# Kernel tuning notes

Hardware: AMD Instinct MI355X
Metric: run time of the kernel (lower is better)

## Reference

```python
import jax, jax.numpy as jnp
import numpy as np

N_SUP, D = 4096, 128
N_CLASSES, SHOTS = 128, 32          # balanced episode: N_SUP = N_CLASSES * SHOTS
N_QUERY = 65536
N_BOOT = 8                          # num_bootstrap_samples


def setup_inputs() -> dict:
    key = jax.random.key(0)
    k_sup, k_q, k_boot = jax.random.split(key, 3)
    support_set_repr = jax.random.normal(k_sup, (N_SUP, D), dtype=jnp.float32)
    # balanced, sorted labels: class c owns contiguous block [c*SHOTS, (c+1)*SHOTS)
    support_labels = (jnp.arange(N_SUP, dtype=jnp.int32) // SHOTS).astype(jnp.int32)
    query_set_repr = jax.random.normal(k_q, (N_QUERY, D), dtype=jnp.float32)
    # externalized torch.randint(0, num_samples, (B, num_samples)) per class
    bootstrap_indices = jax.random.randint(
        k_boot, (N_BOOT, N_CLASSES, SHOTS), 0, SHOTS, dtype=jnp.int32)
    return {
        "support_set_repr": support_set_repr,
        "support_labels": support_labels,
        "query_set_repr": query_set_repr,
        "bootstrap_indices": bootstrap_indices,
    }


def reference(support_set_repr, support_labels, query_set_repr, bootstrap_indices):
    B, C, S = bootstrap_indices.shape
    d = support_set_repr.shape[-1]
    # labels are sorted & balanced (arange // SHOTS), so per-class gather == reshape
    class_repr = support_set_repr.reshape(C, S, d)              # [C, S, D]
    # fused bootstrap gather: [B, C, S, D]
    boot = jnp.take_along_axis(class_repr[None], bootstrap_indices[..., None], axis=2)
    protos = boot.mean(axis=2)                                   # [B, C, D]
    # cdist(q, protos, p=2) via ||q||^2 + ||p||^2 - 2 q.p
    q2 = jnp.sum(query_set_repr * query_set_repr, axis=-1)       # [NQ]
    p2 = jnp.sum(protos * protos, axis=-1)                       # [B, C]
    qp = jnp.einsum('qd,bcd->bqc', query_set_repr, protos)       # [B, NQ, C]
    d2 = q2[None, :, None] + p2[:, None, :] - 2.0 * qp
    dists = jnp.sqrt(jnp.maximum(d2, 0.0))                       # [B, NQ, C]
    # logits = mean over bootstraps of -dists
    return -dists.mean(axis=0)                                   # [NQ, C]
```

## Files before the change

### kernel.cpp

```cpp
#include <hip/hip_runtime.h>
#include <hip/hip_bf16.h>


#define DIM   128
#define NCLS  128
#define SHOTS 32
#define NB    8
#define NQ    65536

using f32x4 = __attribute__((ext_vector_type(4))) float;

__device__ __forceinline__ float fast_sqrt(float x) {
#if __has_builtin(__builtin_amdgcn_sqrtf)
  return __builtin_amdgcn_sqrtf(x);
#else
  return sqrtf(x);
#endif
}

__device__ __forceinline__ long u2l(unsigned x, unsigned y) {
  union { unsigned u[2]; long l; } v; v.u[0] = x; v.u[1] = y; return v.l;
}

__device__ __forceinline__ unsigned pack4_fp8(float a, float b, float c, float d) {
  int r = 0;
  r = __builtin_amdgcn_cvt_pk_fp8_f32(a, b, r, false);
  r = __builtin_amdgcn_cvt_pk_fp8_f32(c, d, r, true);
  return (unsigned)r;
}

__global__ __launch_bounds__(128) void proto_kernel(
    const float* __restrict__ sup, const int* __restrict__ bidx,
    unsigned char* __restrict__ pfrag, float* __restrict__ p2) {
  int bc = blockIdx.x;
  int c  = bc & (NCLS - 1);
  int d  = threadIdx.x;
  __shared__ int   sidx[SHOTS];
  __shared__ float wsum[2];
  if (d < SHOTS) sidx[d] = bidx[bc * SHOTS + d];
  __syncthreads();
  float acc = 0.f;
  const float* base = sup + c * SHOTS * DIM + d;
  #pragma unroll
  for (int s = 0; s < SHOTS; ++s) acc += base[sidx[s] * DIM];
  float proto = acc * (1.0f / 32.0f);

  int b     = bc >> 7;
  int ct    = c >> 4, l15c = c & 15;
  int kiter = d >> 5, quad = (d >> 3) & 3, j = d & 7;
  int lane  = l15c + (quad << 4);
  int addr  = ((b * 8 + ct) * 2 + (kiter >> 1)) * 1024 + lane * 16 + (kiter & 1) * 8 + j;
  int enc   = __builtin_amdgcn_cvt_pk_fp8_f32(-proto, -proto, 0, false);
  pfrag[addr] = (unsigned char)(enc & 0xff);

  float sq = proto * proto;
  #pragma unroll
  for (int off = 32; off > 0; off >>= 1) sq += __shfl_down(sq, off, 64);
  if ((d & 63) == 0) wsum[d >> 6] = sq;
  __syncthreads();
  if (d == 0) p2[bc] = (wsum[0] + wsum[1]) * 0.5f;
}

__global__ __launch_bounds__(256) void dist_kernel(
    const float* __restrict__ q, const uint4* __restrict__ pfrag,
    const float* __restrict__ p2, float* __restrict__ out) {
  int tid  = threadIdx.x;
  int w    = tid >> 6, lane = tid & 63;
  int l15  = lane & 15, quad = lane >> 4;
  int q0   = blockIdx.x << 5;

  __shared__ unsigned char aflds[8 * 512];
  __shared__ float q2s[32];

  {
    int rloc  = w * 8 + (lane >> 3);
    int chunk = lane & 7;
    const float* src = q + (size_t)(q0 + rloc) * DIM + chunk * 16;
    float4 x0 = *reinterpret_cast<const float4*>(src);
    float4 x1 = *reinterpret_cast<const float4*>(src + 4);
    float4 x2 = *reinterpret_cast<const float4*>(src + 8);
    float4 x3 = *reinterpret_cast<const float4*>(src + 12);
    float s = x0.x*x0.x + x0.y*x0.y + x0.z*x0.z + x0.w*x0.w
            + x1.x*x1.x + x1.y*x1.y + x1.z*x1.z + x1.w*x1.w
            + x2.x*x2.x + x2.y*x2.y + x2.z*x2.z + x2.w*x2.w
            + x3.x*x3.x + x3.y*x3.y + x3.z*x3.z + x3.w*x3.w;
    s += __shfl_down(s, 4, 8);
    s += __shfl_down(s, 2, 8);
    s += __shfl_down(s, 1, 8);
    if (chunk == 0) q2s[rloc] = s;

    int mt = rloc >> 4, m = rloc & 15, i = chunk >> 1, h = chunk & 1;
    unsigned char* bse = &aflds[(mt * 4 + i) * 512];
    uint2 g0, g1;
    g0.x = pack4_fp8(x0.x, x0.y, x0.z, x0.w);
    g0.y = pack4_fp8(x1.x, x1.y, x1.z, x1.w);
    g1.x = pack4_fp8(x2.x, x2.y, x2.z, x2.w);
    g1.y = pack4_fp8(x3.x, x3.y, x3.z, x3.w);
    *reinterpret_cast<uint2*>(&bse[(((h * 2 + 0) << 4) + m) * 8]) = g0;
    *reinterpret_cast<uint2*>(&bse[(((h * 2 + 1) << 4) + m) * 8]) = g1;
  }
  __syncthreads();

  long af[2][4];
  #pragma unroll
  for (int mt = 0; mt < 2; ++mt)
    #pragma unroll
    for (int k = 0; k < 4; ++k)
      af[mt][k] = *reinterpret_cast<const long*>(
          &aflds[(mt * 4 + k) * 512 + lane * 8]);

  f32x4 q2r[2];
  #pragma unroll
  for (int mt = 0; mt < 2; ++mt)
    #pragma unroll
    for (int r = 0; r < 4; ++r)
      q2r[mt][r] = q2s[mt * 16 + quad * 4 + r] * 0.5f;

  float p2v[NB][2];
  #pragma unroll
  for (int b = 0; b < NB; ++b)
    #pragma unroll
    for (int jj = 0; jj < 2; ++jj)
      p2v[b][jj] = p2[b * NCLS + (w * 2 + jj) * 16 + l15];

  f32x4 oacc[2][2];
  #pragma unroll
  for (int i = 0; i < 2; ++i)
    #pragma unroll
    for (int jj = 0; jj < 2; ++jj)
      oacc[i][jj] = (f32x4){0.f, 0.f, 0.f, 0.f};

  uint4 bufX[4], bufY[4];

  #define LOAD_B(BUF, B)                                                      \
    {                                                                         \
      _Pragma("unroll")                                                       \
      for (int jj = 0; jj < 2; ++jj) {                                        \
        int ct = w * 2 + jj;                                                  \
        const uint4* bp = pfrag + (size_t)(((B) * 8 + ct) * 2) * 64 + lane;   \
        BUF[jj * 2 + 0] = bp[0];                                              \
        BUF[jj * 2 + 1] = bp[64];                                             \
      }                                                                       \
    }

  #define COMPUTE_B(BUF, B)                                                   \
    {                                                                         \
      _Pragma("unroll")                                                       \
      for (int jj = 0; jj < 2; ++jj) {                                        \
        long b0 = u2l(BUF[jj * 2 + 0].x, BUF[jj * 2 + 0].y);                  \
        long b1 = u2l(BUF[jj * 2 + 0].z, BUF[jj * 2 + 0].w);                  \
        long b2 = u2l(BUF[jj * 2 + 1].x, BUF[jj * 2 + 1].y);                  \
        long b3 = u2l(BUF[jj * 2 + 1].z, BUF[jj * 2 + 1].w);                  \
        f32x4 qp0, qp1;                                                       \
        _Pragma("unroll")                                                     \
        for (int r = 0; r < 4; ++r) {                                         \
          qp0[r] = q2r[0][r] + p2v[B][jj];                                    \
          qp1[r] = q2r[1][r] + p2v[B][jj];                                    \
        }                                                                     \
        qp0 = __builtin_amdgcn_mfma_f32_16x16x32_fp8_fp8(af[0][0], b0, qp0, 0, 0, 0); \
        qp1 = __builtin_amdgcn_mfma_f32_16x16x32_fp8_fp8(af[1][0], b0, qp1, 0, 0, 0); \
        qp0 = __builtin_amdgcn_mfma_f32_16x16x32_fp8_fp8(af[0][1], b1, qp0, 0, 0, 0); \
        qp1 = __builtin_amdgcn_mfma_f32_16x16x32_fp8_fp8(af[1][1], b1, qp1, 0, 0, 0); \
        qp0 = __builtin_amdgcn_mfma_f32_16x16x32_fp8_fp8(af[0][2], b2, qp0, 0, 0, 0); \
        qp1 = __builtin_amdgcn_mfma_f32_16x16x32_fp8_fp8(af[1][2], b2, qp1, 0, 0, 0); \
        qp0 = __builtin_amdgcn_mfma_f32_16x16x32_fp8_fp8(af[0][3], b3, qp0, 0, 0, 0); \
        qp1 = __builtin_amdgcn_mfma_f32_16x16x32_fp8_fp8(af[1][3], b3, qp1, 0, 0, 0); \
        _Pragma("unroll")                                                     \
        for (int r = 0; r < 4; ++r) {                                         \
          oacc[0][jj][r] += fast_sqrt(fmaxf(qp0[r], 0.0f));                   \
          oacc[1][jj][r] += fast_sqrt(fmaxf(qp1[r], 0.0f));                   \
        }                                                                     \
      }                                                                       \
    }

  LOAD_B(bufX, 0)
  #pragma unroll 1
  for (int i = 0; i < NB; i += 2) {
    LOAD_B(bufY, i + 1)
    COMPUTE_B(bufX, i)
    LOAD_B(bufX, (i + 2) & (NB - 1))
    COMPUTE_B(bufY, i + 1)
  }
  #undef LOAD_B
  #undef COMPUTE_B

  #pragma unroll
  for (int mt2 = 0; mt2 < 2; ++mt2)
    #pragma unroll
    for (int jj = 0; jj < 2; ++jj) {
      int col = (w * 2 + jj) * 16 + l15;
      #pragma unroll
      for (int r = 0; r < 4; ++r) {
        int row = q0 + mt2 * 16 + quad * 4 + r;
        out[(size_t)row * NCLS + col] = -0.17677669529663689f * oacc[mt2][jj][r];
      }
    }
}

extern "C" void kernel_launch(void* const* d_in, const int* in_sizes, int n_in,
                              void* d_out, int out_size, void* d_ws, size_t ws_size,
                              hipStream_t stream) {
  const float* sup   = (const float*)d_in[0];
  const float* query = (const float*)d_in[2];
  const int*   bidx  = (const int*)d_in[3];
  float* out = (float*)d_out;

  unsigned char* pfrag = (unsigned char*)d_ws;
  float* p2 = (float*)((char*)d_ws + 256 * 1024);

  proto_kernel<<<NB * NCLS, 128, 0, stream>>>(sup, bidx, pfrag, p2);
  dist_kernel<<<NQ / 32, 256, 0, stream>>>(query, (const uint4*)pfrag, p2, out);
}
```

Before: 113.1 us.

## Drop register double-buffering of prototype fragments and raise occupancy hint

Removes the manual two-buffer prefetch of prototype fragments and the preloaded per-bootstrap p2 array, loading fragments and p2 inside a simple loop over bootstraps. Adds a launch-bounds occupancy hint of 8 blocks per CU so the compiler caps register use. The intent is to lower VGPR pressure and hide load latency through more resident waves rather than software pipelining. The risk is exposed global-load latency per iteration if occupancy does not rise enough.

```diff
diff --git a/kernel.cpp b/kernel.cpp
--- a/kernel.cpp
+++ b/kernel.cpp
@@ -61,7 +61,7 @@
   if (d == 0) p2[bc] = (wsum[0] + wsum[1]) * 0.5f;
 }
 
-__global__ __launch_bounds__(256) void dist_kernel(
+__global__ __launch_bounds__(256, 8) void dist_kernel(
     const float* __restrict__ q, const uint4* __restrict__ pfrag,
     const float* __restrict__ p2, float* __restrict__ out) {
   int tid  = threadIdx.x;
@@ -116,13 +116,6 @@
     for (int r = 0; r < 4; ++r)
       q2r[mt][r] = q2s[mt * 16 + quad * 4 + r] * 0.5f;
 
-  float p2v[NB][2];
-  #pragma unroll
-  for (int b = 0; b < NB; ++b)
-    #pragma unroll
-    for (int jj = 0; jj < 2; ++jj)
-      p2v[b][jj] = p2[b * NCLS + (w * 2 + jj) * 16 + l15];
-
   f32x4 oacc[2][2];
   #pragma unroll
   for (int i = 0; i < 2; ++i)
@@ -130,59 +123,40 @@
     for (int jj = 0; jj < 2; ++jj)
       oacc[i][jj] = (f32x4){0.f, 0.f, 0.f, 0.f};
 
-  uint4 bufX[4], bufY[4];
+  #pragma unroll 1
+  for (int b = 0; b < NB; ++b) {
+    #pragma unroll
+    for (int jj = 0; jj < 2; ++jj) {
+      int ct = w * 2 + jj;
+      const uint4* bp = pfrag + (size_t)((b * 8 + ct) * 2) * 64 + lane;
+      uint4 f0 = bp[0];
+      uint4 f1 = bp[64];
+      float p2b = p2[b * NCLS + ct * 16 + l15];
 
-  #define LOAD_B(BUF, B)                                                      \
-    {                                                                         \
-      _Pragma("unroll")                                                       \
-      for (int jj = 0; jj < 2; ++jj) {                                        \
-        int ct = w * 2 + jj;                                                  \
-        const uint4* bp = pfrag + (size_t)(((B) * 8 + ct) * 2) * 64 + lane;   \
-        BUF[jj * 2 + 0] = bp[0];                                              \
-        BUF[jj * 2 + 1] = bp[64];                                             \
-      }                                                                       \
+      f32x4 qp0, qp1;
+      #pragma unroll
+      for (int r = 0; r < 4; ++r) {
+        qp0[r] = q2r[0][r] + p2b;
+        qp1[r] = q2r[1][r] + p2b;
+      }
+      long b0 = u2l(f0.x, f0.y), b1 = u2l(f0.z, f0.w);
+      long b2 = u2l(f1.x, f1.y), b3 = u2l(f1.z, f1.w);
+      qp0 = __builtin_amdgcn_mfma_f32_16x16x32_fp8_fp8(af[0][0], b0, qp0, 0, 0, 0);
+      qp1 = __builtin_amdgcn_mfma_f32_16x16x32_fp8_fp8(af[1][0], b0, qp1, 0, 0, 0);
+      qp0 = __builtin_amdgcn_mfma_f32_16x16x32_fp8_fp8(af[0][1], b1, qp0, 0, 0, 0);
+      qp1 = __builtin_amdgcn_mfma_f32_16x16x32_fp8_fp8(af[1][1], b1, qp1, 0, 0, 0);
+      qp0 = __builtin_amdgcn_mfma_f32_16x16x32_fp8_fp8(af[0][2], b2, qp0, 0, 0, 0);
+      qp1 = __builtin_amdgcn_mfma_f32_16x16x32_fp8_fp8(af[1][2], b2, qp1, 0, 0, 0);
+      qp0 = __builtin_amdgcn_mfma_f32_16x16x32_fp8_fp8(af[0][3], b3, qp0, 0, 0, 0);
+      qp1 = __builtin_amdgcn_mfma_f32_16x16x32_fp8_fp8(af[1][3], b3, qp1, 0, 0, 0);
+
+      #pragma unroll
+      for (int r = 0; r < 4; ++r) {
+        oacc[0][jj][r] += fast_sqrt(fmaxf(qp0[r], 0.0f));
+        oacc[1][jj][r] += fast_sqrt(fmaxf(qp1[r], 0.0f));
+      }
     }
-
-  #define COMPUTE_B(BUF, B)                                                   \
-    {                                                                         \
-      _Pragma("unroll")                                                       \
-      for (int jj = 0; jj < 2; ++jj) {                                        \
-        long b0 = u2l(BUF[jj * 2 + 0].x, BUF[jj * 2 + 0].y);                  \
-        long b1 = u2l(BUF[jj * 2 + 0].z, BUF[jj * 2 + 0].w);                  \
-        long b2 = u2l(BUF[jj * 2 + 1].x, BUF[jj * 2 + 1].y);                  \
-        long b3 = u2l(BUF[jj * 2 + 1].z, BUF[jj * 2 + 1].w);                  \
-        f32x4 qp0, qp1;                                                       \
-        _Pragma("unroll")                                                     \
-        for (int r = 0; r < 4; ++r) {                                         \
-          qp0[r] = q2r[0][r] + p2v[B][jj];                                    \
-          qp1[r] = q2r[1][r] + p2v[B][jj];                                    \
-        }                                                                     \
-        qp0 = __builtin_amdgcn_mfma_f32_16x16x32_fp8_fp8(af[0][0], b0, qp0, 0, 0, 0); \
-        qp1 = __builtin_amdgcn_mfma_f32_16x16x32_fp8_fp8(af[1][0], b0, qp1, 0, 0, 0); \
-        qp0 = __builtin_amdgcn_mfma_f32_16x16x32_fp8_fp8(af[0][1], b1, qp0, 0, 0, 0); \
-        qp1 = __builtin_amdgcn_mfma_f32_16x16x32_fp8_fp8(af[1][1], b1, qp1, 0, 0, 0); \
-        qp0 = __builtin_amdgcn_mfma_f32_16x16x32_fp8_fp8(af[0][2], b2, qp0, 0, 0, 0); \
-        qp1 = __builtin_amdgcn_mfma_f32_16x16x32_fp8_fp8(af[1][2], b2, qp1, 0, 0, 0); \
-        qp0 = __builtin_amdgcn_mfma_f32_16x16x32_fp8_fp8(af[0][3], b3, qp0, 0, 0, 0); \
-        qp1 = __builtin_amdgcn_mfma_f32_16x16x32_fp8_fp8(af[1][3], b3, qp1, 0, 0, 0); \
-        _Pragma("unroll")                                                     \
-        for (int r = 0; r < 4; ++r) {                                         \
-          oacc[0][jj][r] += fast_sqrt(fmaxf(qp0[r], 0.0f));                   \
-          oacc[1][jj][r] += fast_sqrt(fmaxf(qp1[r], 0.0f));                   \
-        }                                                                     \
-      }                                                                       \
-    }
-
-  LOAD_B(bufX, 0)
-  #pragma unroll 1
-  for (int i = 0; i < NB; i += 2) {
-    LOAD_B(bufY, i + 1)
-    COMPUTE_B(bufX, i)
-    LOAD_B(bufX, (i + 2) & (NB - 1))
-    COMPUTE_B(bufY, i + 1)
   }
-  #undef LOAD_B
-  #undef COMPUTE_B
 
   #pragma unroll
   for (int mt2 = 0; mt2 < 2; ++mt2)
```

Measured after the change: 113.6 us. About the same (+0.5%).
